# Performance work log

Measured on AMD Instinct MI355X. Metric: run time of the kernel, lower is better.

The kernel has to match this reference:

```python
import jax, jax.numpy as jnp
import numpy as np

POOL = 4
SCALE = 1.0 / 16.0
B, C, H, W = 64, 256, 36, 36
NC = POOL * POOL           # 16 correlation channels
RED = 4                    # SE reduction
INTER = NC // 2            # non-local inter channels = 8


def _hat_cumint(t):
    # integral of hat kernel max(0,1-|s|) over (-inf, t]
    t = jnp.clip(t, -1.0, 1.0)
    return jnp.where(t < 0.0, 0.5 * (t + 1.0) ** 2, 1.0 - 0.5 * (1.0 - t) ** 2)


def _axis_weights(lo, hi, n):
    # lo, hi: (B, P) bin edges in feature coords -> (B, P, n) exact integral
    # of the bilinear (hat) basis of each integer sample i over [lo, hi].
    i = jnp.arange(n, dtype=lo.dtype)
    return _hat_cumint(hi[..., None] - i) - _hat_cumint(lo[..., None] - i)


def prroi_pool(feat, rois_xyxy, pool, scale):
    # Precise RoI Pooling: analytic integral of bilinear interpolation per bin.
    Bn, Cn, Hn, Wn = feat.shape
    x1 = rois_xyxy[:, 0] * scale
    y1 = rois_xyxy[:, 1] * scale
    x2 = rois_xyxy[:, 2] * scale
    y2 = rois_xyxy[:, 3] * scale
    bw = (x2 - x1) / pool
    bh = (y2 - y1) / pool
    k = jnp.arange(pool, dtype=feat.dtype)
    ax = x1[:, None] + k * bw[:, None]
    bx = ax + bw[:, None]
    ay = y1[:, None] + k * bh[:, None]
    by = ay + bh[:, None]
    Wx = _axis_weights(ax, bx, Wn)   # (B, P, W)
    Wy = _axis_weights(ay, by, Hn)   # (B, P, H)
    pooled = jnp.einsum('bchw,bph,bqw->bcpq', feat, Wy, Wx)
    area = (bw * bh)[:, None, None, None]
    return jnp.where(area > 0, pooled / jnp.maximum(area, 1e-12), 0.0)


def setup_inputs() -> dict:
    key = jax.random.key(0)
    ks = jax.random.split(key, 12)
    feat1 = jax.random.normal(ks[0], (B, C, H, W), jnp.float32)
    feat2 = jax.random.normal(ks[1], (B, C, H, W), jnp.float32)
    # valid (x, y, w, h) boxes inside a 576px image
    xy = jax.random.uniform(ks[2], (B, 2), jnp.float32, 0.0, 416.0)
    wh = jax.random.uniform(ks[3], (B, 2), jnp.float32, 32.0, 160.0)
    bb1 = jnp.concatenate([xy, wh], axis=1)[None]  # (1, B, 4)

    def conv_init(k, shape):  # normal(0, sqrt(2/(kh*kw*out)))
        n = shape[0]  # 1x1 convs: kh*kw*out_ch = out_ch
        return jax.random.normal(k, shape, jnp.float32) * np.sqrt(2.0 / n)

    se_w1 = conv_init(ks[4], (NC // RED, NC))
    se_w2 = conv_init(ks[5], (NC, NC // RED))
    nl_theta_w = conv_init(ks[6], (INTER, NC))
    nl_phi_w = conv_init(ks[7], (INTER, NC))
    nl_g_w = conv_init(ks[8], (INTER, NC))
    nl_W_w = conv_init(ks[9], (NC, INTER))
    zi = jnp.zeros((INTER,), jnp.float32)
    zc = jnp.zeros((NC,), jnp.float32)
    return {
        'feat1': feat1, 'feat2': feat2, 'bb1': bb1,
        'se_w1': se_w1, 'se_w2': se_w2,
        'nl_theta_w': nl_theta_w, 'nl_theta_b': zi,
        'nl_phi_w': nl_phi_w, 'nl_phi_b': zi,
        'nl_g_w': nl_g_w, 'nl_g_b': zi,
        'nl_W_w': nl_W_w, 'nl_W_b': zc,
    }


def reference(feat1, feat2, bb1, se_w1, se_w2, nl_theta_w, nl_theta_b,
              nl_phi_w, nl_phi_b, nl_g_w, nl_g_b, nl_W_w, nl_W_b):
    boxes = bb1[0]  # (B, 4) xywh
    xyxy = jnp.concatenate([boxes[:, :2], boxes[:, :2] + boxes[:, 2:4]], axis=1)
    ker = prroi_pool(feat1, xyxy, POOL, SCALE)          # (B, C, P, P)
    Bn, Cn, Hn, Wn = feat2.shape
    kflat = ker.reshape(Bn, Cn, NC)
    # pixel_corr: per-sample 1x1 conv == batched GEMM
    corr = jnp.einsum('bchw,bck->bkhw', feat2, kflat)   # (B, 16, H, W)
    # SE channel attention
    s = corr.mean(axis=(2, 3))                          # (B, 16)
    s = jax.nn.sigmoid(jax.nn.relu(s @ se_w1.T) @ se_w2.T)
    x = corr * s[:, :, None, None]
    # Non-local (embedded gaussian) spatial attention
    xf = x.reshape(Bn, NC, Hn * Wn)                     # (B, 16, N)
    theta = jnp.einsum('oc,bcn->bno', nl_theta_w, xf) + nl_theta_b     # (B, N, 8)
    phi = jnp.einsum('oc,bcn->bon', nl_phi_w, xf) + nl_phi_b[:, None]  # (B, 8, N)
    g = jnp.einsum('oc,bcn->bno', nl_g_w, xf) + nl_g_b                 # (B, N, 8)
    attn = jax.nn.softmax(jnp.einsum('bno,bom->bnm', theta, phi), axis=-1)
    y = jnp.einsum('bnm,bmo->bno', attn, g)             # (B, N, 8)
    z = jnp.einsum('co,bno->bcn', nl_W_w, y) + nl_W_b[:, None]
    return z.reshape(Bn, NC, Hn, Wn) + x
```

## Files before the change

### kernel.cpp

```cpp
#include <hip/hip_runtime.h>
#include <cmath>

#define NB 64
#define NCC 256
#define NH 36
#define NW 36
#define NHW 1296
#define NK 16
#define NI 8
#define SC (1.0f/16.0f)
#define LOG2E 1.4426950408889634f
#define NPAD 1312

typedef __attribute__((ext_vector_type(16))) float f32x16;
typedef __attribute__((ext_vector_type(4)))  float f32x4;
typedef __attribute__((ext_vector_type(4)))  short s16x4;
typedef __attribute__((ext_vector_type(8)))  unsigned short u16x8;
typedef __attribute__((ext_vector_type(2)))  unsigned int u32x2;

__device__ __forceinline__ float hatc(float t){
  t = fminf(fmaxf(t, -1.0f), 1.0f);
  float a = 1.0f + t, bq = 1.0f - t;
  return (t < 0.0f) ? 0.5f*a*a : 1.0f - 0.5f*bq*bq;
}

__device__ __forceinline__ unsigned short bf16rn(float f){
  unsigned int u = __builtin_bit_cast(unsigned int, f);
  return (unsigned short)((u + 0x7FFFu + ((u >> 16) & 1u)) >> 16);
}
__device__ __forceinline__ float bf16tof(unsigned short h){
  unsigned int u = ((unsigned int)h) << 16;
  return __builtin_bit_cast(float, u);
}

__global__ __launch_bounds__(256) void k_prpool(const float* __restrict__ feat1,
    const float* __restrict__ bb1, float* __restrict__ kflat){
  int blk = blockIdx.x;
  int b = blk >> 6, cg = blk & 63;
  int t = threadIdx.x, w = t >> 6, lane = t & 63;
  int c = cg*4 + w;
  __shared__ float4 wY4[36];
  __shared__ float  wXp[36*5];
  float bx = bb1[b*4+0], by = bb1[b*4+1], bwv = bb1[b*4+2], bhv = bb1[b*4+3];
  float x1 = bx*SC, y1 = by*SC;
  float binw = bwv*SC*0.25f, binh = bhv*SC*0.25f;
  if (t < 36){
    float fi = (float)t;
    float4 r;
    r.x = hatc(y1 + 1.0f*binh - fi) - hatc(y1 + 0.0f*binh - fi);
    r.y = hatc(y1 + 2.0f*binh - fi) - hatc(y1 + 1.0f*binh - fi);
    r.z = hatc(y1 + 3.0f*binh - fi) - hatc(y1 + 2.0f*binh - fi);
    r.w = hatc(y1 + 4.0f*binh - fi) - hatc(y1 + 3.0f*binh - fi);
    wY4[t] = r;
  } else if (t < 72){
    int i = t - 36;
    float fi = (float)i;
    wXp[i*5+0] = hatc(x1 + 1.0f*binw - fi) - hatc(x1 + 0.0f*binw - fi);
    wXp[i*5+1] = hatc(x1 + 2.0f*binw - fi) - hatc(x1 + 1.0f*binw - fi);
    wXp[i*5+2] = hatc(x1 + 3.0f*binw - fi) - hatc(x1 + 2.0f*binw - fi);
    wXp[i*5+3] = hatc(x1 + 4.0f*binw - fi) - hatc(x1 + 3.0f*binw - fi);
  }
  __syncthreads();
  f32x4 acc4[4];
  #pragma unroll
  for (int p=0;p<4;p++) acc4[p] = (f32x4){0,0,0,0};
  const float4* fp4 = (const float4*)(feat1 + ((size_t)(b*256+c))*NHW);

  auto body = [&](float4 v, int px){
    #pragma unroll
    for (int j=0;j<4;j++){
      int p = px + j;
      int h = p/36, x = p - h*36;
      float vj = (j==0)?v.x:(j==1)?v.y:(j==2)?v.z:v.w;
      float4 wy = wY4[h];
      f32x4 wxv = {wXp[x*5+0], wXp[x*5+1], wXp[x*5+2], wXp[x*5+3]};
      f32x4 a0 = {vj*wy.x, vj*wy.x, vj*wy.x, vj*wy.x};
      f32x4 a1 = {vj*wy.y, vj*wy.y, vj*wy.y, vj*wy.y};
      f32x4 a2 = {vj*wy.z, vj*wy.z, vj*wy.z, vj*wy.z};
      f32x4 a3 = {vj*wy.w, vj*wy.w, vj*wy.w, vj*wy.w};
      acc4[0] = __builtin_elementwise_fma(a0, wxv, acc4[0]);
      acc4[1] = __builtin_elementwise_fma(a1, wxv, acc4[1]);
      acc4[2] = __builtin_elementwise_fma(a2, wxv, acc4[2]);
      acc4[3] = __builtin_elementwise_fma(a3, wxv, acc4[3]);
    }
  };

  #pragma unroll
  for (int i=0;i<5;i++){
    int f4i = i*64 + lane;
    float4 v = fp4[f4i];
    body(v, f4i*4);
  }
  if (lane < 4){
    int f4i = 320 + lane;
    float4 v = fp4[f4i];
    body(v, f4i*4);
  }
  float accf[16];
  #pragma unroll
  for (int p=0;p<4;p++){
    accf[p*4+0]=acc4[p].x; accf[p*4+1]=acc4[p].y;
    accf[p*4+2]=acc4[p].z; accf[p*4+3]=acc4[p].w;
  }
  #pragma unroll
  for (int k=0;k<16;k++){
    float a = accf[k];
    #pragma unroll
    for (int off=32; off>0; off>>=1) a += __shfl_down(a, off);
    accf[k] = a;
  }
  if (lane == 0){
    float area = binw*binh;
    float ia = (area > 0.0f) ? 1.0f/fmaxf(area,1e-12f) : 0.0f;
    float4* kp = (float4*)(kflat + ((size_t)(b*256+c))*16);
    kp[0] = make_float4(accf[0]*ia, accf[1]*ia, accf[2]*ia, accf[3]*ia);
    kp[1] = make_float4(accf[4]*ia, accf[5]*ia, accf[6]*ia, accf[7]*ia);
    kp[2] = make_float4(accf[8]*ia, accf[9]*ia, accf[10]*ia, accf[11]*ia);
    kp[3] = make_float4(accf[12]*ia, accf[13]*ia, accf[14]*ia, accf[15]*ia);
  }
}

__global__ __launch_bounds__(512) void k_corr(const float* __restrict__ feat2,
    const float* __restrict__ kflat, float* __restrict__ corr,
    float* __restrict__ partial_se){
  int blk = blockIdx.x;
  int b = blk / 6, ch = blk - b*6;
  int t = threadIdx.x, w = t >> 6, lane = t & 63;
  int px0 = ch*216;
  __shared__ float par[4][16][216];

  int wu = __builtin_amdgcn_readfirstlane(w);
  int c0 = wu*32;
  int l4 = (lane < 54) ? lane : 53;

  f32x4 acc[16];
  #pragma unroll
  for (int k=0;k<16;k++) acc[k] = (f32x4){0,0,0,0};

  const float* f2base = feat2 + (size_t)b*NCC*NHW + px0 + l4*4;
  const float* kfb = kflat + (size_t)b*4096;
  #pragma unroll 4
  for (int c = c0; c < c0+32; ++c){
    f32x4 r = *(const f32x4*)(f2base + (size_t)c*NHW);
    f32x16 kf = *(const f32x16*)(kfb + c*16);
    #pragma unroll
    for (int k=0;k<16;k++){
      f32x4 kv = {kf[k], kf[k], kf[k], kf[k]};
      acc[k] = __builtin_elementwise_fma(r, kv, acc[k]);
    }
  }

  if (w >= 4){
    #pragma unroll
    for (int k=0;k<16;k++)
      *(f32x4*)&par[w-4][k][l4*4] = acc[k];
  }
  __syncthreads();
  if (w < 4){
    #pragma unroll
    for (int k=0;k<16;k++){
      f32x4 tmp = *(const f32x4*)&par[w][k][l4*4];
      *(f32x4*)&par[w][k][l4*4] = tmp + acc[k];
    }
  }
  __syncthreads();
  int k = (w<<1) | (lane>>5);
  int j0 = lane & 31;
  float se_r = 0.0f;
  float* cp = corr + (size_t)b*NK*NHW + (size_t)k*NHW + px0;
  for (int jj=j0; jj<54; jj+=32){
    f32x4 s = *(const f32x4*)&par[0][k][jj*4];
    s += *(const f32x4*)&par[1][k][jj*4];
    s += *(const f32x4*)&par[2][k][jj*4];
    s += *(const f32x4*)&par[3][k][jj*4];
    *(f32x4*)(cp + jj*4) = s;
    se_r += (s.x+s.y) + (s.z+s.w);
  }
  #pragma unroll
  for (int off=16; off>0; off>>=1) se_r += __shfl_down(se_r, off, 32);
  if (j0 == 0)
    partial_se[(size_t)blk*16 + k] = se_r;
}

__global__ __launch_bounds__(256) void k_tpg(const float* __restrict__ corr,
    const float* __restrict__ partial_se,
    const float* __restrict__ w1, const float* __restrict__ w2,
    const float* __restrict__ tw, const float* __restrict__ tb,
    const float* __restrict__ pw, const float* __restrict__ pb,
    const float* __restrict__ gw, const float* __restrict__ gb,
    float* __restrict__ sscale,
    unsigned short* __restrict__ thetaX, unsigned short* __restrict__ phiX,
    unsigned short* __restrict__ gT){
  int blk = blockIdx.x;
  int b = blk/6, ch = blk - b*6;
  int t = threadIdx.x;
  __shared__ float Wt[128], Wp[128], Wg[128], Bz[24], Ss[16], sS[16], sR[4];
  if (t < 128){ Wt[t]=tw[t]; Wp[t]=pw[t]; Wg[t]=gw[t]; }
  if (t < 8){ Bz[t]=tb[t]; Bz[8+t]=pb[t]; Bz[16+t]=gb[t]; }
  if (t >= 128 && t < 144){
    int q = t - 128;
    float a = 0.f;
    #pragma unroll
    for (int c2=0; c2<6; c2++) a += partial_se[(size_t)(b*6+c2)*16 + q];
    sS[q] = a * (1.0f/1296.0f);
  }
  __syncthreads();
  if (t < 4){
    float a=0.f;
    #pragma unroll
    for (int k=0;k<16;k++) a += sS[k]*w1[t*16+k];
    sR[t] = fmaxf(a, 0.f);
  }
  __syncthreads();
  if (t < 16){
    float a=0.f;
    #pragma unroll
    for (int j=0;j<4;j++) a += sR[j]*w2[t*4+j];
    float gsc = 1.0f/(1.0f+__expf(-a));
    Ss[t] = gsc;
    if (ch == 0) sscale[b*16+t] = gsc;
  }
  __syncthreads();
  int n = ch*256 + t;
  if (n >= NHW) return;
  float x[16];
  const float* cp = corr + (size_t)b*NK*NHW + n;
  #pragma unroll
  for (int c=0;c<16;c++) x[c] = cp[(size_t)c*NHW] * Ss[c];
  float th[8], ph[8], gg[8];
  #pragma unroll
  for (int o=0;o<8;o++){
    float a=Bz[o], p2=Bz[8+o], gq=Bz[16+o];
    #pragma unroll
    for (int c=0;c<16;c++){
      a  += Wt[o*16+c]*x[c];
      p2 += Wp[o*16+c]*x[c];
      gq += Wg[o*16+c]*x[c];
    }
    th[o]=a*LOG2E; ph[o]=p2; gg[o]=gq;
  }
  unsigned short tH[8], tL[8], pH[8], pL[8];
  #pragma unroll
  for (int o=0;o<8;o++){
    unsigned short hh = bf16rn(th[o]);
    tH[o] = hh; tL[o] = bf16rn(th[o] - bf16tof(hh));
    unsigned short ph2 = bf16rn(ph[o]);
    pH[o] = ph2; pL[o] = bf16rn(ph[o] - bf16tof(ph2));
  }
  {
    u16x8* tp = (u16x8*)(thetaX + ((size_t)b*NPAD + n)*16);
    tp[0] = (u16x8){tH[0],tH[1],tH[2],tH[3], tL[0],tL[1],tL[2],tL[3]};
    tp[1] = (u16x8){tH[4],tH[5],tH[6],tH[7], tL[4],tL[5],tL[6],tL[7]};
    u16x8* pp = (u16x8*)(phiX + ((size_t)b*NPAD + n)*16);
    pp[0] = (u16x8){pH[0],pH[1],pH[2],pH[3], pL[0],pL[1],pL[2],pL[3]};
    pp[1] = (u16x8){pH[4],pH[5],pH[6],pH[7], pL[4],pL[5],pL[6],pL[7]};
  }
  #pragma unroll
  for (int o=0;o<8;o++)
    gT[((size_t)b*16 + o)*NPAD + n] = bf16rn(gg[o]);
  gT[((size_t)b*16 + 8)*NPAD + n] = 0x3F80;
}

__global__ __launch_bounds__(128) void k_attn_part(
    const unsigned short* __restrict__ thetaX, const unsigned short* __restrict__ phiX,
    const unsigned short* __restrict__ gT,
    float* __restrict__ mpart, float* __restrict__ Ypart){
  int blk = blockIdx.x;
  int b = blk / 82, rem = blk - b*82;
  int qb = rem >> 1, kh = rem & 1;
  int t = threadIdx.x, w = t >> 6, lane = t & 63;
  int h = lane >> 5, r31 = lane & 31;
  __shared__ float smm[2][32];
  __shared__ float sY[16][64];
  __shared__ float yl[32][12];

  const unsigned short* thx = thetaX + (size_t)b*NPAD*16;
  const unsigned short* phx = phiX   + (size_t)b*NPAD*16;

  s16x4 Bh, Bl;
  {
    const s16x4* tp = (const s16x4*)(thx + ((size_t)(qb*32 + r31))*16 + h*8);
    Bh = tp[0]; Bl = tp[1];
  }

  int kbeg = kh ? 21 : 0;
  int kend = kh ? 41 : 21;
  int kmid = kh ? 31 : 11;
  int kt0 = w ? kmid : kbeg;
  int ktN = w ? kend : kmid;

  float m = -1e30f;
  {
    const unsigned short* prow = phx + (size_t)(kt0*32 + r31)*16 + h*8;
    for (int kt = kt0; kt < ktN; ++kt){
      const s16x4* pr = (const s16x4*)prow;
      s16x4 Ah = pr[0];
      f32x16 S = __builtin_amdgcn_mfma_f32_32x32x8bf16_1k(Ah, Bh, (f32x16)(0.0f), 0, 0, 0);
      if (kt != 40){
        float a0 = fmaxf(S[0],S[1]),  a1 = fmaxf(S[2],S[3]);
        float a2 = fmaxf(S[4],S[5]),  a3 = fmaxf(S[6],S[7]);
        float a4 = fmaxf(S[8],S[9]),  a5 = fmaxf(S[10],S[11]);
        float a6 = fmaxf(S[12],S[13]),a7 = fmaxf(S[14],S[15]);
        float b0 = fmaxf(a0,a1), b1 = fmaxf(a2,a3);
        float b2 = fmaxf(a4,a5), b3 = fmaxf(a6,a7);
        m = fmaxf(m, fmaxf(fmaxf(b0,b1), fmaxf(b2,b3)));
      } else {
        float a0 = fmaxf(S[0],S[1]), a1 = fmaxf(S[2],S[3]);
        float a2 = fmaxf(S[4],S[5]), a3 = fmaxf(S[6],S[7]);
        m = fmaxf(m, fmaxf(fmaxf(a0,a1), fmaxf(a2,a3)));
      }
      prow += 512;
    }
  }
  m = fmaxf(m, __shfl_xor(m, 32));
  if (h == 0) smm[w][r31] = m;
  __syncthreads();
  m = fmaxf(smm[0][r31], smm[1][r31]);
  if (w == 0 && h == 0)
    mpart[((size_t)((b*41 + qb)*2 + kh))*32 + r31] = m;

  f32x16 Y = (f32x16)(0.0f);
  int colc = (r31 < 9) ? r31 : 0;
  const unsigned short* gb2 = gT + ((size_t)b*16 + colc)*NPAD;

  {
    const unsigned short* prow = phx + (size_t)(kt0*32 + r31)*16 + h*8;
    const unsigned short* vrow = gb2 + kt0*32;
    for (int kt = kt0; kt < ktN; ++kt){
      const s16x4* pr = (const s16x4*)prow;
      s16x4 Ah = pr[0], Al = pr[1];
      f32x16 S = __builtin_amdgcn_mfma_f32_32x32x8bf16_1k(Ah, Bl, (f32x16)(0.0f), 0, 0, 0);
      S = __builtin_amdgcn_mfma_f32_32x32x8bf16_1k(Al, Bh, S, 0, 0, 0);
      S = __builtin_amdgcn_mfma_f32_32x32x8bf16_1k(Ah, Bh, S, 0, 0, 0);
      if (kt == 40){
        #pragma unroll
        for (int r=8;r<16;r++) S[r] = -1e30f;
      }
      float p[16];
      #pragma unroll
      for (int r=0;r<16;r++) p[r] = __builtin_amdgcn_exp2f(S[r] - m);
      unsigned int c[8];
      #pragma unroll
      for (int i=0;i<8;i++){
        unsigned int cc;
        asm("v_cvt_pk_bf16_f32 %0, %1, %2" : "=v"(cc) : "v"(p[2*i]), "v"(p[2*i+1]));
        c[i] = cc;
      }
      const s16x4* vr = (const s16x4*)(vrow + h*4);
      #pragma unroll
      for (int mf=0; mf<4; ++mf){
        s16x4 Ap = __builtin_bit_cast(s16x4, (u32x2){c[2*mf], c[2*mf+1]});
        s16x4 Vb = vr[mf*2];
        Y = __builtin_amdgcn_mfma_f32_32x32x8bf16_1k(Ap, Vb, Y, 0, 0, 0);
      }
      prow += 512;
      vrow += 32;
    }
  }

  if (w == 1){
    #pragma unroll
    for (int r=0;r<16;r++) sY[r][lane] = Y[r];
  }
  __syncthreads();
  if (w == 0){
    #pragma unroll
    for (int r=0;r<16;r++) Y[r] += sY[r][lane];
    if (r31 < 9){
      #pragma unroll
      for (int r=0;r<16;r++){
        int q = (r&3) + 8*(r>>2) + 4*h;
        yl[q][r31] = Y[r];
      }
    }
  }
  __syncthreads();

  float* yp = Ypart + (size_t)((b*41 + qb)*2 + kh)*288;
  for (int i = t; i < 288; i += 128){
    int q = i / 9, c2 = i - q*9;
    yp[i] = yl[q][c2];
  }
}

__global__ __launch_bounds__(128) void k_attn_fin(
    const float* __restrict__ mpart, const float* __restrict__ Ypart,
    const float* __restrict__ corr, const float* __restrict__ sscale,
    const float* __restrict__ Ww, const float* __restrict__ Wb,
    float* __restrict__ out){
  int blk = blockIdx.x;
  int b = blk / 41, qb = blk - b*41;
  int t = threadIdx.x;
  __shared__ float yl[32][9];
  __shared__ float cf0[32], cf1[32];
  size_t p2 = (size_t)(b*41 + qb)*2;
  if (t < 32){
    float m0 = mpart[p2*32 + t];
    float m1 = mpart[(p2+1)*32 + t];
    float M = fmaxf(m0, m1);
    cf0[t] = __builtin_amdgcn_exp2f(m0 - M);
    cf1[t] = __builtin_amdgcn_exp2f(m1 - M);
  }
  __syncthreads();
  const float* y0 = Ypart + p2*288;
  const float* y1 = Ypart + (p2+1)*288;
  for (int i = t; i < 288; i += 128){
    int q = i / 9;
    ((float*)yl)[i] = y0[i]*cf0[q] + y1[i]*cf1[q];
  }
  __syncthreads();

  int q = t & 31, cg = t >> 5;
  int n = qb*32 + q;
  if (n < NHW){
    float il = 1.0f / yl[q][8];
    float yv[8];
    #pragma unroll
    for (int o=0;o<8;o++) yv[o] = yl[q][o] * il;
    const float* cp = corr + (size_t)b*NK*NHW + n;
    const float* ss = sscale + b*16;
    float* op = out + (size_t)b*NK*NHW + n;
    #pragma unroll
    for (int i=0;i<4;i++){
      int c2 = cg*4 + i;
      float z = Wb[c2];
      #pragma unroll
      for (int o=0;o<8;o++) z += Ww[c2*8+o]*yv[o];
      op[(size_t)c2*NHW] = z + cp[(size_t)c2*NHW]*ss[c2];
    }
  }
}

extern "C" void kernel_launch(void* const* d_in, const int* in_sizes, int n_in,
                              void* d_out, int out_size, void* d_ws, size_t ws_size,
                              hipStream_t stream){
  const float* feat1 = (const float*)d_in[0];
  const float* feat2 = (const float*)d_in[1];
  const float* bb1   = (const float*)d_in[2];
  const float* se_w1 = (const float*)d_in[3];
  const float* se_w2 = (const float*)d_in[4];
  const float* tw    = (const float*)d_in[5];
  const float* tb    = (const float*)d_in[6];
  const float* pw    = (const float*)d_in[7];
  const float* pb    = (const float*)d_in[8];
  const float* gw    = (const float*)d_in[9];
  const float* gb    = (const float*)d_in[10];
  const float* Ww    = (const float*)d_in[11];
  const float* Wb    = (const float*)d_in[12];
  float* out = (float*)d_out;

  float* ws = (float*)d_ws;
  float* kflat      = ws;
  float* corr       = kflat + 64*256*16;
  float* partial_se = corr + (size_t)64*16*1296;
  float* sscale     = partial_se + 64*6*16;
  unsigned short* thetaX = (unsigned short*)(sscale + 64*16);
  unsigned short* phiX   = thetaX + (size_t)64*NPAD*16;
  unsigned short* gT     = phiX   + (size_t)64*NPAD*16;
  float* mpart = (float*)(gT + (size_t)64*16*NPAD);
  float* Ypart = mpart + (size_t)64*41*2*32;

  hipLaunchKernelGGL(k_prpool, dim3(64*64), dim3(256), 0, stream, feat1, bb1, kflat);
  hipLaunchKernelGGL(k_corr, dim3(64*6), dim3(512), 0, stream, feat2, kflat, corr, partial_se);
  hipLaunchKernelGGL(k_tpg, dim3(64*6), dim3(256), 0, stream, corr, partial_se,
                     se_w1, se_w2, tw, tb, pw, pb, gw, gb, sscale, thetaX, phiX, gT);
  hipLaunchKernelGGL(k_attn_part, dim3(64*82), dim3(128), 0, stream,
                     thetaX, phiX, gT, mpart, Ypart);
  hipLaunchKernelGGL(k_attn_fin, dim3(64*41), dim3(128), 0, stream,
                     mpart, Ypart, corr, sscale, Ww, Wb, out);
}
```

Baseline: 109.7 us.

## Use online softmax in attention partial kernel, dropping separate max pass

Removes the first pass over the key tiles that computed the row maximum. The running max is now updated per tile, with the accumulator rescaled by an exp2 correction factor as each tile arrives (online softmax). The final MFMA operands are swapped so the output is transposed and only 5 accumulator registers are live, which shrinks the rescale work and the shared-memory reduction. This saves one MFMA and load pass per tile in exchange for per-tile cross-lane shuffles, an extra exp and a dependency on the running max.

```diff
diff --git a/kernel.cpp b/kernel.cpp
--- a/kernel.cpp
+++ b/kernel.cpp
@@ -271,7 +271,7 @@
   int t = threadIdx.x, w = t >> 6, lane = t & 63;
   int h = lane >> 5, r31 = lane & 31;
   __shared__ float smm[2][32];
-  __shared__ float sY[16][64];
+  __shared__ float sY[5][64];
   __shared__ float yl[32][12];
 
   const unsigned short* thx = thetaX + (size_t)b*NPAD*16;
@@ -290,35 +290,6 @@
   int ktN = w ? kend : kmid;
 
   float m = -1e30f;
-  {
-    const unsigned short* prow = phx + (size_t)(kt0*32 + r31)*16 + h*8;
-    for (int kt = kt0; kt < ktN; ++kt){
-      const s16x4* pr = (const s16x4*)prow;
-      s16x4 Ah = pr[0];
-      f32x16 S = __builtin_amdgcn_mfma_f32_32x32x8bf16_1k(Ah, Bh, (f32x16)(0.0f), 0, 0, 0);
-      if (kt != 40){
-        float a0 = fmaxf(S[0],S[1]),  a1 = fmaxf(S[2],S[3]);
-        float a2 = fmaxf(S[4],S[5]),  a3 = fmaxf(S[6],S[7]);
-        float a4 = fmaxf(S[8],S[9]),  a5 = fmaxf(S[10],S[11]);
-        float a6 = fmaxf(S[12],S[13]),a7 = fmaxf(S[14],S[15]);
-        float b0 = fmaxf(a0,a1), b1 = fmaxf(a2,a3);
-        float b2 = fmaxf(a4,a5), b3 = fmaxf(a6,a7);
-        m = fmaxf(m, fmaxf(fmaxf(b0,b1), fmaxf(b2,b3)));
-      } else {
-        float a0 = fmaxf(S[0],S[1]), a1 = fmaxf(S[2],S[3]);
-        float a2 = fmaxf(S[4],S[5]), a3 = fmaxf(S[6],S[7]);
-        m = fmaxf(m, fmaxf(fmaxf(a0,a1), fmaxf(a2,a3)));
-      }
-      prow += 512;
-    }
-  }
-  m = fmaxf(m, __shfl_xor(m, 32));
-  if (h == 0) smm[w][r31] = m;
-  __syncthreads();
-  m = fmaxf(smm[0][r31], smm[1][r31]);
-  if (w == 0 && h == 0)
-    mpart[((size_t)((b*41 + qb)*2 + kh))*32 + r31] = m;
-
   f32x16 Y = (f32x16)(0.0f);
   int colc = (r31 < 9) ? r31 : 0;
   const unsigned short* gb2 = gT + ((size_t)b*16 + colc)*NPAD;
@@ -336,9 +307,22 @@
         #pragma unroll
         for (int r=8;r<16;r++) S[r] = -1e30f;
       }
+      float a0 = fmaxf(S[0],S[1]),  a1 = fmaxf(S[2],S[3]);
+      float a2 = fmaxf(S[4],S[5]),  a3 = fmaxf(S[6],S[7]);
+      float a4 = fmaxf(S[8],S[9]),  a5 = fmaxf(S[10],S[11]);
+      float a6 = fmaxf(S[12],S[13]),a7 = fmaxf(S[14],S[15]);
+      float b0 = fmaxf(a0,a1), b1 = fmaxf(a2,a3);
+      float b2 = fmaxf(a4,a5), b3 = fmaxf(a6,a7);
+      float tm = fmaxf(fmaxf(b0,b1), fmaxf(b2,b3));
+      tm = fmaxf(tm, __shfl_xor(tm, 32));
+      float mn = fmaxf(m, tm);
+      float cf = __builtin_amdgcn_exp2f(m - mn);
+      m = mn;
       float p[16];
       #pragma unroll
       for (int r=0;r<16;r++) p[r] = __builtin_amdgcn_exp2f(S[r] - m);
+      #pragma unroll
+      for (int r=0;r<5;r++) Y[r] *= cf;
       unsigned int c[8];
       #pragma unroll
       for (int i=0;i<8;i++){
@@ -351,27 +335,34 @@
       for (int mf=0; mf<4; ++mf){
         s16x4 Ap = __builtin_bit_cast(s16x4, (u32x2){c[2*mf], c[2*mf+1]});
         s16x4 Vb = vr[mf*2];
-        Y = __builtin_amdgcn_mfma_f32_32x32x8bf16_1k(Ap, Vb, Y, 0, 0, 0);
+        Y = __builtin_amdgcn_mfma_f32_32x32x8bf16_1k(Vb, Ap, Y, 0, 0, 0);
       }
       prow += 512;
       vrow += 32;
     }
   }
 
+  if (h == 0) smm[w][r31] = m;
+  __syncthreads();
+  float M = fmaxf(smm[0][r31], smm[1][r31]);
+  float cfw = __builtin_amdgcn_exp2f(m - M);
+  #pragma unroll
+  for (int r=0;r<5;r++) Y[r] *= cfw;
+  if (w == 0 && h == 0)
+    mpart[((size_t)((b*41 + qb)*2 + kh))*32 + r31] = M;
   if (w == 1){
     #pragma unroll
-    for (int r=0;r<16;r++) sY[r][lane] = Y[r];
+    for (int r=0;r<5;r++) sY[r][lane] = Y[r];
   }
   __syncthreads();
   if (w == 0){
     #pragma unroll
-    for (int r=0;r<16;r++) Y[r] += sY[r][lane];
-    if (r31 < 9){
-      #pragma unroll
-      for (int r=0;r<16;r++){
-        int q = (r&3) + 8*(r>>2) + 4*h;
-        yl[q][r31] = Y[r];
-      }
+    for (int r=0;r<5;r++) Y[r] += sY[r][lane];
+    if (h == 0){
+      yl[r31][0]=Y[0]; yl[r31][1]=Y[1]; yl[r31][2]=Y[2]; yl[r31][3]=Y[3];
+      yl[r31][8]=Y[4];
+    } else {
+      yl[r31][4]=Y[0]; yl[r31][5]=Y[1]; yl[r31][6]=Y[2]; yl[r31][7]=Y[3];
     }
   }
   __syncthreads();
```

After: 101.3 us (median of 2 runs). 1.08x faster.
